# Kernel optimization log

Measured on AMD Instinct MI355X. Metric: run time of the kernel, lower is better.

## Reference

```python
import jax, jax.numpy as jnp
import numpy as np

DIM = 1024
HEADS = 16
DH = 64            # dim // heads
LOCAL_HEADS = 8
WINDOW = 128
NEG = -jnp.finfo(jnp.float32).max


def _look_around_kv(z, pad_value):
    # z: (b, h, nw, w, d) -> (b, h, nw, 3w, d); backward=1, forward=1 window
    nw = z.shape[2]
    zp = jnp.pad(z, ((0, 0), (0, 0), (1, 1), (0, 0), (0, 0)), constant_values=pad_value)
    return jnp.concatenate([zp[:, :, i:i + nw] for i in range(3)], axis=3)


def _local_attention(q, k, v, valid):
    # q,k,v: (b, h, t, d); valid: (b, t) True = keep (module passes ~input_mask)
    b, h, t, d = q.shape
    nw = t // WINDOW
    bucket = lambda z: z.reshape(b, h, nw, WINDOW, d)
    bq, bk, bv = bucket(q), bucket(k), bucket(v)
    bk = _look_around_kv(bk, 0.0)
    bv = _look_around_kv(bv, 0.0)
    # key position indices with -1 padding for out-of-range windows
    t_idx = jnp.arange(t, dtype=jnp.int32).reshape(nw, WINDOW)
    tp = jnp.pad(t_idx, ((1, 1), (0, 0)), constant_values=-1)
    bq_k = jnp.concatenate([tp[i:i + nw] for i in range(3)], axis=1)  # (nw, 3w)
    oob = (bq_k == -1)[None, None, :, None, :]                        # (1,1,nw,1,3w)
    # input mask pair: mq & mk
    vm = valid.reshape(b, nw, WINDOW)
    vmp = jnp.pad(vm, ((0, 0), (1, 1), (0, 0)), constant_values=False)
    vmk = jnp.concatenate([vmp[:, i:i + nw] for i in range(3)], axis=2)  # (b, nw, 3w)
    pair = vm[:, None, :, :, None] & vmk[:, None, :, None, :]            # (b,1,nw,w,3w)
    dots = jnp.einsum('bhnwd,bhnkd->bhnwk', bq, bk) * (d ** -0.5)
    dots = jnp.where(oob, NEG, dots)
    dots = jnp.where(pair, dots, NEG)
    attn = jax.nn.softmax(dots, axis=-1)
    out = jnp.einsum('bhnwk,bhnkd->bhnwd', attn, bv)
    return out.reshape(b, h, t, d)


def _linear_attn(q, k, v, valid):
    # q,k,v: (b, h, t, d); valid: (b, t) True = keep
    d = q.shape[-1]
    m = valid[:, None, :, None]
    k = jnp.where(m, k, NEG)
    v = jnp.where(m, v, 0.0)
    q = jax.nn.softmax(q, axis=-1) * (d ** -0.5)
    k = jax.nn.softmax(k, axis=-2)
    context = jnp.einsum('bhnd,bhne->bhde', k, v)
    return jnp.einsum('bhnd,bhde->bhne', q, context)


def setup_inputs() -> dict:
    key = jax.random.key(0)
    ks = jax.random.split(key, 7)
    b, t = 2, 4096
    x = jax.random.normal(ks[0], (b, t, DIM), dtype=jnp.float32)
    input_mask = jax.random.bernoulli(ks[1], 0.1, (b, t))  # True = padded token
    s = DIM ** -0.5
    Wq = jax.random.normal(ks[2], (DIM, HEADS * DH), jnp.float32) * s
    Wk = jax.random.normal(ks[3], (DIM, HEADS * DH), jnp.float32) * s
    Wv = jax.random.normal(ks[4], (DIM, HEADS * DH), jnp.float32) * s
    Wo = jax.random.normal(ks[5], (HEADS * DH, DIM), jnp.float32) * s
    bo = jax.random.normal(ks[6], (DIM,), jnp.float32) * 0.01
    return {"x": x, "input_mask": input_mask, "Wq": Wq, "Wk": Wk, "Wv": Wv, "Wo": Wo, "bo": bo}


def reference(x, input_mask, Wq, Wk, Wv, Wo, bo):
    b, t, _ = x.shape
    split_heads = lambda z: z.reshape(b, t, HEADS, DH).transpose(0, 2, 1, 3)
    q = split_heads(x @ Wq)
    k = split_heads(x @ Wk)
    v = split_heads(x @ Wv)
    valid = ~input_mask
    lq, gq = q[:, :LOCAL_HEADS], q[:, LOCAL_HEADS:]
    lk, gk = k[:, :LOCAL_HEADS], k[:, LOCAL_HEADS:]
    lv, gv = v[:, :LOCAL_HEADS], v[:, LOCAL_HEADS:]
    local_out = _local_attention(lq, lk, lv, valid)
    global_out = _linear_attn(gq, gk, gv, valid)
    attn = jnp.concatenate([local_out, global_out], axis=1)  # (b, h, t, d)
    attn = attn.transpose(0, 2, 1, 3).reshape(b, t, HEADS * DH)
    return attn @ Wo + bo
```

## Files before the change

kernel.cpp:

```cpp
#include <hip/hip_runtime.h>
#include <cstdint>
#include <cfloat>
#include <math.h>

typedef __bf16 bf16_t;
typedef __bf16 bf16x8 __attribute__((ext_vector_type(8)));
typedef __bf16 bf16x4 __attribute__((ext_vector_type(4)));
typedef float  f32x4  __attribute__((ext_vector_type(4)));
typedef unsigned int u32;

#define NEGF (-3.4028234663852886e38f)

static __device__ __forceinline__ f32x4 mfma16(bf16x8 a, bf16x8 b, f32x4 c) {
  return __builtin_amdgcn_mfma_f32_16x16x32_bf16(a, b, c, 0, 0, 0);
}
static __device__ __forceinline__ void gload_lds16(const bf16_t* g, bf16_t* l) {
  __builtin_amdgcn_global_load_lds((const __attribute__((address_space(1))) void*)g,
                                   (__attribute__((address_space(3))) void*)l, 16, 0, 0);
}

__global__ __launch_bounds__(256) void k_prep_all(const float* __restrict__ x,
                                                  const uint8_t* __restrict__ mraw,
                                                  const float* __restrict__ Wq,
                                                  const float* __restrict__ Wk,
                                                  const float* __restrict__ Wv,
                                                  const float* __restrict__ Wo,
                                                  bf16_t* __restrict__ xb,
                                                  bf16_t* __restrict__ WT,
                                                  bf16_t* __restrict__ WoT,
                                                  uint8_t* __restrict__ valid) {
  int bid = blockIdx.x;
  int tid = threadIdx.x;
  if (bid < 8192) {
    int i = bid * 256 + tid;
    float4 v = ((const float4*)x)[i];
    bf16x4 o = { (bf16_t)v.x, (bf16_t)v.y, (bf16_t)v.z, (bf16_t)v.w };
    *(bf16x4*)(xb + (size_t)i * 4) = o;
  } else if (bid < 12288) {
    __shared__ float tile[32][33];
    int zz = bid - 8192;
    int z = zz >> 10, rem = zz & 1023;
    int bx = rem & 31, by = rem >> 5;
    const float* src = (z == 0) ? Wq : (z == 1) ? Wk : (z == 2) ? Wv : Wo;
    bf16_t* dst = (z < 3) ? (WT + (size_t)z * 1024 * 1024) : WoT;
    int x0 = bx * 32, y0 = by * 32;
    int tx = tid & 31, ty = tid >> 5;
    #pragma unroll
    for (int j = 0; j < 32; j += 8)
      tile[ty + j][tx] = src[(size_t)(y0 + ty + j) * 1024 + x0 + tx];
    __syncthreads();
    #pragma unroll
    for (int j = 0; j < 32; j += 8)
      dst[(size_t)(x0 + ty + j) * 1024 + y0 + tx] = (bf16_t)tile[tx][ty + j];
  } else {
    __shared__ int f1, f3;
    if (tid == 0) { f1 = 0; f3 = 0; }
    __syncthreads();
    int l1 = 0, l3 = 0;
    for (int i = tid; i < 8192; i += 256) {
      uint8_t v = mraw[i];
      if (v) { int r = i & 3; if (r == 1 || r == 2) l1 = 1; if (r == 3) l3 = 1; }
    }
    if (l1) atomicOr(&f1, 1);
    if (l3) atomicOr(&f3, 1);
    __syncthreads();
    int layout = f1 ? 0 : (f3 ? 2 : 1);
    for (int i = tid; i < 8192; i += 256) {
      bool m;
      if (layout == 0)      m = mraw[i] != 0;
      else if (layout == 1) m = ((const int*)mraw)[i] != 0;
      else                  m = ((const float*)mraw)[i] != 0.0f;
      valid[i] = m ? (uint8_t)0 : (uint8_t)1;
    }
  }
}

template<bool OUT_BF16>
__global__ __launch_bounds__(256, 2) void k_gemm(const bf16_t* __restrict__ A,
                                                 const bf16_t* __restrict__ Bt,
                                                 void* __restrict__ Cout,
                                                 const float* __restrict__ bias,
                                                 int M, int N, int K) {
  __shared__ __align__(16) uint8_t shmem[34816];
  bf16_t* As = (bf16_t*)shmem;
  bf16_t* Bs = As + 128 * 64;
  int id  = blockIdx.x;
  int seq = id >> 3;
  int nbg = seq >> 6, inner = seq & 63;
  int mb = ((id & 7) << 3) + (inner >> 3);
  int nb = (nbg << 3) + (inner & 7);

  const int tid = threadIdx.x;
  const int lane = tid & 63, wv = tid >> 6;
  const int c = lane & 15, g = lane >> 4;
  const size_t m0 = (size_t)mb * 128, n0 = (size_t)nb * 128;
  const int wm = (wv >> 1) * 64, wn = (wv & 1) * 64;

  f32x4 zero = {0.f, 0.f, 0.f, 0.f};
  f32x4 acc[4][4];
  #pragma unroll
  for (int m = 0; m < 4; ++m)
    #pragma unroll
    for (int n = 0; n < 4; ++n) acc[m][n] = zero;

  for (int kt = 0; kt < K; kt += 64) {
    if (kt) __syncthreads();
    #pragma unroll
    for (int p = 0; p < 4; ++p) {
      int seg = p * 256 + tid;
      int r = seg >> 3, s = seg & 7;
      int sc = (s ^ (r & 7)) * 8;
      gload_lds16(A + (m0 + r) * (size_t)K + kt + sc, As + seg * 8);
    }
    #pragma unroll
    for (int p = 0; p < 4; ++p) {
      int seg = p * 256 + tid;
      int r = seg >> 3, s = seg & 7;
      int sc = (s ^ (r & 7)) * 8;
      gload_lds16(Bt + (n0 + r) * (size_t)K + kt + sc, Bs + seg * 8);
    }
    __syncthreads();
    #pragma unroll
    for (int kk = 0; kk < 2; ++kk) {
      bf16x8 af[4], bfv[4];
      #pragma unroll
      for (int m = 0; m < 4; ++m) {
        int row = wm + m * 16 + c;
        int sl = (g + 4 * kk) ^ (row & 7);
        af[m] = *(const bf16x8*)(As + row * 64 + sl * 8);
      }
      #pragma unroll
      for (int n = 0; n < 4; ++n) {
        int row = wn + n * 16 + c;
        int sl = (g + 4 * kk) ^ (row & 7);
        bfv[n] = *(const bf16x8*)(Bs + row * 64 + sl * 8);
      }
      #pragma unroll
      for (int m = 0; m < 4; ++m)
        #pragma unroll
        for (int n = 0; n < 4; ++n)
          acc[m][n] = mfma16(af[m], bfv[n], acc[m][n]);
    }
  }

  __syncthreads();
  if (OUT_BF16) {
    bf16_t* L = (bf16_t*)shmem;
    #pragma unroll
    for (int m = 0; m < 4; ++m)
      #pragma unroll
      for (int n = 0; n < 4; ++n)
        #pragma unroll
        for (int i = 0; i < 4; ++i)
          L[(wm + m * 16 + 4 * g + i) * 136 + wn + n * 16 + c] = (bf16_t)acc[m][n][i];
    __syncthreads();
    bf16_t* C = (bf16_t*)Cout;
    #pragma unroll
    for (int p = 0; p < 8; ++p) {
      int idx = p * 2048 + tid * 8;
      int row = idx >> 7, col = idx & 127;
      bf16x8 v = *(const bf16x8*)(L + row * 136 + col);
      *(bf16x8*)(C + (m0 + row) * (size_t)N + n0 + col) = v;
    }
  } else {
    float* C = (float*)Cout;
    float* L = (float*)shmem;
    #pragma unroll
    for (int half = 0; half < 2; ++half) {
      if (half) __syncthreads();
      if ((wv >> 1) == half) {
        #pragma unroll
        for (int m = 0; m < 4; ++m)
          #pragma unroll
          for (int n = 0; n < 4; ++n)
            #pragma unroll
            for (int i = 0; i < 4; ++i)
              L[(m * 16 + 4 * g + i) * 132 + wn + n * 16 + c] = acc[m][n][i];
      }
      __syncthreads();
      #pragma unroll
      for (int p = 0; p < 8; ++p) {
        int lin = p * 1024 + tid * 4;
        int row = lin >> 7, col = lin & 127;
        float4 v = *(const float4*)(L + row * 132 + col);
        float4 bv = *(const float4*)(bias + n0 + col);
        v.x += bv.x; v.y += bv.y; v.z += bv.z; v.w += bv.w;
        *(float4*)(C + (m0 + half * 64 + row) * (size_t)N + n0 + col) = v;
      }
    }
  }
}

__global__ __launch_bounds__(512) void k_attn(const bf16_t* __restrict__ qkv,
                                              const uint8_t* __restrict__ valid,
                                              bf16_t* __restrict__ attn,
                                              float* __restrict__ ctxp,
                                              float* __restrict__ sump) {
  __shared__ __align__(16) uint8_t smem[50688];
  int bid = blockIdx.x;
  int tid = threadIdx.x;

  if (bid < 512) {
    bf16_t* Ks = (bf16_t*)smem;
    bf16_t* VT = (bf16_t*)smem;
    uint8_t* s_key = smem + 50176;
    uint8_t* s_q   = smem + 50560;

    int w = bid & 31, h = (bid >> 5) & 7, b = bid >> 8;
    const int lane = tid & 63, wv = tid >> 6;
    const int c = lane & 15, g = lane >> 4;
    const int tkbase = (w - 1) * 128;

    #pragma unroll
    for (int p = 0; p < 6; ++p) {
      int seg = p * 512 + tid;
      int r = seg >> 3, s = seg & 7;
      int tk = tkbase + r;
      bf16x8 v8 = { (bf16_t)0.f,(bf16_t)0.f,(bf16_t)0.f,(bf16_t)0.f,
                    (bf16_t)0.f,(bf16_t)0.f,(bf16_t)0.f,(bf16_t)0.f };
      if ((unsigned)tk < 4096u)
        v8 = *(const bf16x8*)(qkv + (size_t)(b * 4096 + tk) * 3072 + 1024 + h * 64 + s * 8);
      *(bf16x8*)(Ks + r * 64 + ((s ^ (r & 7)) * 8)) = v8;
    }
    if (tid < 384) {
      int tk = tkbase + tid;
      s_key[tid] = ((unsigned)tk < 4096u) ? valid[b * 4096 + tk] : (uint8_t)0;
    }
    if (tid < 128) s_q[tid] = valid[b * 4096 + w * 128 + tid];
    __syncthreads();

    int m0 = wv * 16;
    bf16x8 qa0, qa1;
    {
      const bf16_t* qrow = qkv + (size_t)(b * 4096 + w * 128 + m0 + c) * 3072 + h * 64;
      qa0 = *(const bf16x8*)(qrow + g * 8);
      qa1 = *(const bf16x8*)(qrow + 32 + g * 8);
    }
    f32x4 zero = {0.f, 0.f, 0.f, 0.f};
    f32x4 acc[24];
    #pragma unroll
    for (int nt = 0; nt < 24; ++nt) acc[nt] = zero;
    #pragma unroll
    for (int nt = 0; nt < 24; ++nt) {
      int n = nt * 16 + c;
      bf16x8 k0 = *(const bf16x8*)(Ks + n * 64 + ((g       ^ (n & 7)) * 8));
      bf16x8 k1 = *(const bf16x8*)(Ks + n * 64 + (((g + 4) ^ (n & 7)) * 8));
      acc[nt] = mfma16(k0, qa0, acc[nt]);
      acc[nt] = mfma16(k1, qa1, acc[nt]);
    }
    __syncthreads();

    {
      int e = tid & 63, tg = tid >> 6;
      #pragma unroll 8
      for (int j = 0; j < 48; ++j) {
        int r = tg * 48 + j;
        int tk = tkbase + r;
        bf16_t v = (bf16_t)0.f;
        if ((unsigned)tk < 4096u)
          v = qkv[(size_t)(b * 4096 + tk) * 3072 + 2048 + h * 64 + e];
        VT[e * 392 + r] = v;
      }
    }

    bool qv = s_q[m0 + c] != 0;
    #pragma unroll
    for (int nt = 0; nt < 24; ++nt) {
      u32 kv4 = *(const u32*)(s_key + nt * 16 + 4 * g);
      #pragma unroll
      for (int i = 0; i < 4; ++i) {
        bool kv = ((kv4 >> (8 * i)) & 255u) != 0u;
        acc[nt][i] = (qv && kv) ? acc[nt][i] * 0.125f : NEGF;
      }
    }
    float mx = NEGF;
    #pragma unroll
    for (int nt = 0; nt < 24; ++nt)
      #pragma unroll
      for (int i = 0; i < 4; ++i) mx = fmaxf(mx, acc[nt][i]);
    mx = fmaxf(mx, __shfl_xor(mx, 16, 64));
    mx = fmaxf(mx, __shfl_xor(mx, 32, 64));

    const int srcA = ((lane >> 4) & 1) * 32 + (lane & 15);
    const int srcB = srcA + 16;
    union Pk2 { bf16x4 h; uint2 u; };
    union Pk4 { uint4 u; bf16x8 h; };
    uint4 paU[12];
    #pragma unroll
    for (int ks = 0; ks < 12; ++ks) paU[ks] = make_uint4(0, 0, 0, 0);
    float sum = 0.f;
    #pragma unroll
    for (int nt = 0; nt < 24; ++nt) {
      Pk2 pk;
      #pragma unroll
      for (int i = 0; i < 4; ++i) {
        float e = __expf(acc[nt][i] - mx);
        sum += e;
        pk.h[i] = (bf16_t)e;
      }
      u32 a0 = (u32)__shfl((int)pk.u.x, srcA, 64);
      u32 a1 = (u32)__shfl((int)pk.u.y, srcA, 64);
      u32 b0 = (u32)__shfl((int)pk.u.x, srcB, 64);
      u32 b1 = (u32)__shfl((int)pk.u.y, srcB, 64);
      bool take = ((g >> 1) == (nt & 1));
      int ks = nt >> 1;
      paU[ks].x = take ? a0 : paU[ks].x;
      paU[ks].y = take ? a1 : paU[ks].y;
      paU[ks].z = take ? b0 : paU[ks].z;
      paU[ks].w = take ? b1 : paU[ks].w;
    }
    sum += __shfl_xor(sum, 16, 64);
    sum += __shfl_xor(sum, 32, 64);
    float inv = 1.f / sum;
    float invq[4];
    #pragma unroll
    for (int i = 0; i < 4; ++i) invq[i] = __shfl(inv, 4 * g + i, 64);
    __syncthreads();

    f32x4 o[4];
    #pragma unroll
    for (int n = 0; n < 4; ++n) o[n] = zero;
    #pragma unroll
    for (int ks = 0; ks < 12; ++ks) {
      Pk4 pa; pa.u = paU[ks];
      #pragma unroll
      for (int n = 0; n < 4; ++n) {
        bf16x8 vb = *(const bf16x8*)(VT + (n * 16 + c) * 392 + ks * 32 + g * 8);
        o[n] = mfma16(pa.h, vb, o[n]);
      }
    }
    size_t obase = (size_t)(b * 4096 + w * 128 + m0) * 1024 + h * 64;
    #pragma unroll
    for (int n = 0; n < 4; ++n)
      #pragma unroll
      for (int i = 0; i < 4; ++i)
        attn[obase + (size_t)(4 * g + i) * 1024 + n * 16 + c] = (bf16_t)(o[n][i] * invq[i]);
  } else {
    int bid2 = bid - 512;
    int tc = bid2 & 15, h = (bid2 >> 4) & 7, b = bid2 >> 7;
    float* sk = (float*)smem;
    float* sv = sk + 64 * 64;
    float a00=0,a01=0,a02=0,a03=0,a10=0,a11=0,a12=0,a13=0;
    float a20=0,a21=0,a22=0,a23=0,a30=0,a31=0,a32=0,a33=0;
    float s0=0, s1=0, s2=0, s3=0;
    int dg = tid >> 4, eg = tid & 15;
    for (int ch = 0; ch < 4; ++ch) {
      int t0 = tc * 256 + ch * 64;
      __syncthreads();
      {
        int idx = tid;
        int r = idx >> 3, ss = idx & 7;
        int gt = b * 4096 + t0 + r;
        bool vld = valid[gt] != 0;
        bf16x8 k8 = *(const bf16x8*)(qkv + (size_t)gt * 3072 + 1024 + (8 + h) * 64 + ss * 8);
        bf16x8 v8 = *(const bf16x8*)(qkv + (size_t)gt * 3072 + 2048 + (8 + h) * 64 + ss * 8);
        #pragma unroll
        for (int j = 0; j < 8; ++j) {
          int dd = ss * 8 + j;
          sk[r * 64 + dd] = vld ? __expf((float)k8[j]) : 0.f;
          sv[r * 64 + dd] = vld ? (float)v8[j] : 0.f;
        }
      }
      __syncthreads();
      if (tid < 256) {
        #pragma unroll 4
        for (int r = 0; r < 64; ++r) {
          float4 a = *(const float4*)(sk + r * 64 + dg * 4);
          float4 v = *(const float4*)(sv + r * 64 + eg * 4);
          a00 += a.x*v.x; a01 += a.x*v.y; a02 += a.x*v.z; a03 += a.x*v.w;
          a10 += a.y*v.x; a11 += a.y*v.y; a12 += a.y*v.z; a13 += a.y*v.w;
          a20 += a.z*v.x; a21 += a.z*v.y; a22 += a.z*v.z; a23 += a.z*v.w;
          a30 += a.w*v.x; a31 += a.w*v.y; a32 += a.w*v.z; a33 += a.w*v.w;
          s0 += a.x; s1 += a.y; s2 += a.z; s3 += a.w;
        }
      }
    }
    if (tid < 256) {
      float* dst = ctxp + (size_t)((b * 8 + h) * 16 + tc) * 4096 + (dg * 4) * 64 + eg * 4;
      *(float4*)(dst + 0)   = make_float4(a00, a01, a02, a03);
      *(float4*)(dst + 64)  = make_float4(a10, a11, a12, a13);
      *(float4*)(dst + 128) = make_float4(a20, a21, a22, a23);
      *(float4*)(dst + 192) = make_float4(a30, a31, a32, a33);
      if (eg == 0)
        *(float4*)(sump + (size_t)((b * 8 + h) * 16 + tc) * 64 + dg * 4) = make_float4(s0, s1, s2, s3);
    }
  }
}

__global__ __launch_bounds__(256) void k_ctx2(const float* __restrict__ ctxp,
                                              const float* __restrict__ sump,
                                              bf16_t* __restrict__ ctxT) {
  int bh = blockIdx.x;
  int tid = threadIdx.x;
  __shared__ float inv[64];
  if (tid < 64) {
    float s = 0.f;
    #pragma unroll
    for (int tc = 0; tc < 16; ++tc)
      s += sump[(size_t)(bh * 16 + tc) * 64 + tid];
    inv[tid] = 1.f / s;
  }
  __syncthreads();
  for (int p = 0; p < 16; ++p) {
    int lin = p * 256 + tid;
    int d = lin >> 6, e = lin & 63;
    float s = 0.f;
    #pragma unroll
    for (int tc = 0; tc < 16; ++tc)
      s += ctxp[(size_t)(bh * 16 + tc) * 4096 + lin];
    s *= inv[d];
    ctxT[(size_t)bh * 4096 + e * 64 + d] = (bf16_t)s;
  }
}

__global__ __launch_bounds__(256) void k_linout(const bf16_t* __restrict__ qkv,
                                                const bf16_t* __restrict__ ctxT,
                                                bf16_t* __restrict__ attn) {
  int bid = blockIdx.x;
  int tb2 = bid & 15, hg = (bid >> 4) & 7, b = bid >> 7;
  int tid = threadIdx.x;
  __shared__ bf16_t qs[256 * 72];
  __shared__ bf16_t cT[64 * 72];
  {
    int t = tb2 * 256 + tid;
    const bf16_t* qrow = qkv + (size_t)(b * 4096 + t) * 3072 + (8 + hg) * 64;
    float x[64];
    #pragma unroll
    for (int s8 = 0; s8 < 8; ++s8) {
      bf16x8 q8 = *(const bf16x8*)(qrow + s8 * 8);
      #pragma unroll
      for (int j = 0; j < 8; ++j) x[s8 * 8 + j] = (float)q8[j];
    }
    float m = x[0];
    #pragma unroll
    for (int i = 1; i < 64; ++i) m = fmaxf(m, x[i]);
    float sum = 0.f;
    #pragma unroll
    for (int i = 0; i < 64; ++i) { x[i] = __expf(x[i] - m); sum += x[i]; }
    float sc = 0.125f / sum;
    #pragma unroll
    for (int s8 = 0; s8 < 8; ++s8) {
      bf16x8 o8;
      #pragma unroll
      for (int j = 0; j < 8; ++j) o8[j] = (bf16_t)(x[s8 * 8 + j] * sc);
      *(bf16x8*)(qs + tid * 72 + s8 * 8) = o8;
    }
  }
  for (int idx = tid; idx < 512; idx += 256) {
    int r = idx >> 3, s = idx & 7;
    *(bf16x8*)(cT + r * 72 + s * 8) =
      *(const bf16x8*)(ctxT + (size_t)(b * 8 + hg) * 4096 + r * 64 + s * 8);
  }
  __syncthreads();
  int lane = tid & 63, wvv = tid >> 6;
  int c = lane & 15, g = lane >> 4;
  int m0w = wvv * 64;
  f32x4 zero = {0.f, 0.f, 0.f, 0.f};
  f32x4 acc[4][4];
  #pragma unroll
  for (int m = 0; m < 4; ++m)
    #pragma unroll
    for (int n = 0; n < 4; ++n) acc[m][n] = zero;
  #pragma unroll
  for (int kk = 0; kk < 2; ++kk) {
    bf16x8 af[4], bfv[4];
    #pragma unroll
    for (int m = 0; m < 4; ++m)
      af[m] = *(const bf16x8*)(qs + (m0w + m * 16 + c) * 72 + kk * 32 + g * 8);
    #pragma unroll
    for (int n = 0; n < 4; ++n)
      bfv[n] = *(const bf16x8*)(cT + (n * 16 + c) * 72 + kk * 32 + g * 8);
    #pragma unroll
    for (int m = 0; m < 4; ++m)
      #pragma unroll
      for (int n = 0; n < 4; ++n)
        acc[m][n] = mfma16(af[m], bfv[n], acc[m][n]);
  }
  size_t obase = (size_t)(b * 4096 + tb2 * 256 + m0w) * 1024 + (8 + hg) * 64;
  #pragma unroll
  for (int m = 0; m < 4; ++m)
    #pragma unroll
    for (int n = 0; n < 4; ++n)
      #pragma unroll
      for (int i = 0; i < 4; ++i)
        attn[obase + (size_t)(m * 16 + 4 * g + i) * 1024 + n * 16 + c] = (bf16_t)acc[m][n][i];
}

extern "C" void kernel_launch(void* const* d_in, const int* in_sizes, int n_in,
                              void* d_out, int out_size, void* d_ws, size_t ws_size,
                              hipStream_t stream) {
  const float*   x    = (const float*)d_in[0];
  const uint8_t* mraw = (const uint8_t*)d_in[1];
  const float*   Wq   = (const float*)d_in[2];
  const float*   Wk   = (const float*)d_in[3];
  const float*   Wv   = (const float*)d_in[4];
  const float*   Wo   = (const float*)d_in[5];
  const float*   bo   = (const float*)d_in[6];
  uint8_t* ws = (uint8_t*)d_ws;

  uint8_t* valid = ws;
  bf16_t*  xb    = (bf16_t*)(ws + 8192);
  bf16_t*  WT    = (bf16_t*)(ws + 16785408);
  bf16_t*  WoT   = (bf16_t*)(ws + 23076864);
  bf16_t*  qkv   = (bf16_t*)(ws + 25174016);
  bf16_t*  attn  = (bf16_t*)(ws + 75505664);
  float*   ctxp  = (float*)(ws + 8192);
  float*   sump  = (float*)(ws + 4202496);
  bf16_t*  ctxT  = (bf16_t*)(ws + 4268032);

  k_prep_all<<<12289, 256, 0, stream>>>(x, mraw, Wq, Wk, Wv, Wo, xb, WT, WoT, valid);
  k_gemm<true><<<1536, 256, 0, stream>>>(xb, WT, (void*)qkv, nullptr, 8192, 3072, 1024);
  k_attn<<<768, 512, 0, stream>>>(qkv, valid, attn, ctxp, sump);
  k_ctx2<<<16, 256, 0, stream>>>(ctxp, sump, ctxT);
  k_linout<<<256, 256, 0, stream>>>(qkv, ctxT, attn);
  k_gemm<false><<<512, 256, 0, stream>>>(attn, WoT, d_out, bo, 8192, 1024, 1024);
}
```

Before: 207.2 us.

## Use MFMA for linear-attention context partials and vectorize V transpose loads

The global-head branch now stores exp(K) and V as transposed bf16 tiles in shared memory and computes the K^T V context partial with bf16 MFMA instead of scalar fp32 FMAs. It processes 128-token chunks using all 512 threads rather than 64-token chunks with half the threads. The local branch loads V with 16-byte vector reads before scattering into the transposed LDS tile, replacing scalar per-element loads. The cost is precision: exp(K) is rounded to bf16, and the transposed scalar LDS writes may cause bank conflicts.

```diff
diff --git a/kernel.cpp b/kernel.cpp
--- a/kernel.cpp
+++ b/kernel.cpp
@@ -199,6 +199,9 @@
   __shared__ __align__(16) uint8_t smem[50688];
   int bid = blockIdx.x;
   int tid = threadIdx.x;
+  const int lane = tid & 63, wv = tid >> 6;
+  const int c = lane & 15, g = lane >> 4;
+  f32x4 zero = {0.f, 0.f, 0.f, 0.f};
 
   if (bid < 512) {
     bf16_t* Ks = (bf16_t*)smem;
@@ -207,8 +210,6 @@
     uint8_t* s_q   = smem + 50560;
 
     int w = bid & 31, h = (bid >> 5) & 7, b = bid >> 8;
-    const int lane = tid & 63, wv = tid >> 6;
-    const int c = lane & 15, g = lane >> 4;
     const int tkbase = (w - 1) * 128;
 
     #pragma unroll
@@ -236,7 +237,6 @@
       qa0 = *(const bf16x8*)(qrow + g * 8);
       qa1 = *(const bf16x8*)(qrow + 32 + g * 8);
     }
-    f32x4 zero = {0.f, 0.f, 0.f, 0.f};
     f32x4 acc[24];
     #pragma unroll
     for (int nt = 0; nt < 24; ++nt) acc[nt] = zero;
@@ -250,17 +250,18 @@
     }
     __syncthreads();
 
-    {
-      int e = tid & 63, tg = tid >> 6;
-      #pragma unroll 8
-      for (int j = 0; j < 48; ++j) {
-        int r = tg * 48 + j;
-        int tk = tkbase + r;
-        bf16_t v = (bf16_t)0.f;
-        if ((unsigned)tk < 4096u)
-          v = qkv[(size_t)(b * 4096 + tk) * 3072 + 2048 + h * 64 + e];
-        VT[e * 392 + r] = v;
-      }
+    #pragma unroll
+    for (int p = 0; p < 6; ++p) {
+      int seg = p * 512 + tid;
+      int r = seg >> 3, s = seg & 7;
+      int tk = tkbase + r;
+      bf16x8 v8 = { (bf16_t)0.f,(bf16_t)0.f,(bf16_t)0.f,(bf16_t)0.f,
+                    (bf16_t)0.f,(bf16_t)0.f,(bf16_t)0.f,(bf16_t)0.f };
+      if ((unsigned)tk < 4096u)
+        v8 = *(const bf16x8*)(qkv + (size_t)(b * 4096 + tk) * 3072 + 2048 + h * 64 + s * 8);
+      #pragma unroll
+      for (int j = 0; j < 8; ++j)
+        VT[(s * 8 + j) * 392 + r] = v8[j];
     }
 
     bool qv = s_q[m0 + c] != 0;
@@ -338,52 +339,61 @@
   } else {
     int bid2 = bid - 512;
     int tc = bid2 & 15, h = (bid2 >> 4) & 7, b = bid2 >> 7;
-    float* sk = (float*)smem;
-    float* sv = sk + 64 * 64;
-    float a00=0,a01=0,a02=0,a03=0,a10=0,a11=0,a12=0,a13=0;
-    float a20=0,a21=0,a22=0,a23=0,a30=0,a31=0,a32=0,a33=0;
-    float s0=0, s1=0, s2=0, s3=0;
-    int dg = tid >> 4, eg = tid & 15;
-    for (int ch = 0; ch < 4; ++ch) {
-      int t0 = tc * 256 + ch * 64;
+    bf16_t* eKT = (bf16_t*)smem;
+    bf16_t* vT  = (bf16_t*)(smem + 17408);
+    int dt = wv >> 1, et2 = (wv & 1) * 2;
+    f32x4 acc2[2];
+    acc2[0] = zero; acc2[1] = zero;
+    float rowsum = 0.f;
+    int rsrow = wv * 8 + (lane >> 3);
+    int rscol = (lane & 7) * 16;
+    for (int ch = 0; ch < 2; ++ch) {
       __syncthreads();
-      {
-        int idx = tid;
+      #pragma unroll
+      for (int p = 0; p < 2; ++p) {
+        int idx = p * 512 + tid;
         int r = idx >> 3, ss = idx & 7;
-        int gt = b * 4096 + t0 + r;
+        int gt = b * 4096 + tc * 256 + ch * 128 + r;
         bool vld = valid[gt] != 0;
         bf16x8 k8 = *(const bf16x8*)(qkv + (size_t)gt * 3072 + 1024 + (8 + h) * 64 + ss * 8);
         bf16x8 v8 = *(const bf16x8*)(qkv + (size_t)gt * 3072 + 2048 + (8 + h) * 64 + ss * 8);
         #pragma unroll
         for (int j = 0; j < 8; ++j) {
           int dd = ss * 8 + j;
-          sk[r * 64 + dd] = vld ? __expf((float)k8[j]) : 0.f;
-          sv[r * 64 + dd] = vld ? (float)v8[j] : 0.f;
+          eKT[dd * 136 + r] = vld ? (bf16_t)__expf((float)k8[j]) : (bf16_t)0.f;
+          vT [dd * 136 + r] = vld ? v8[j] : (bf16_t)0.f;
         }
       }
       __syncthreads();
-      if (tid < 256) {
-        #pragma unroll 4
-        for (int r = 0; r < 64; ++r) {
-          float4 a = *(const float4*)(sk + r * 64 + dg * 4);
-          float4 v = *(const float4*)(sv + r * 64 + eg * 4);
-          a00 += a.x*v.x; a01 += a.x*v.y; a02 += a.x*v.z; a03 += a.x*v.w;
-          a10 += a.y*v.x; a11 += a.y*v.y; a12 += a.y*v.z; a13 += a.y*v.w;
-          a20 += a.z*v.x; a21 += a.z*v.y; a22 += a.z*v.z; a23 += a.z*v.w;
-          a30 += a.w*v.x; a31 += a.w*v.y; a32 += a.w*v.z; a33 += a.w*v.w;
-          s0 += a.x; s1 += a.y; s2 += a.z; s3 += a.w;
+      #pragma unroll
+      for (int ks = 0; ks < 4; ++ks) {
+        bf16x8 af = *(const bf16x8*)(eKT + (dt * 16 + c) * 136 + ks * 32 + g * 8);
+        #pragma unroll
+        for (int n = 0; n < 2; ++n) {
+          bf16x8 bf = *(const bf16x8*)(vT + ((et2 + n) * 16 + c) * 136 + ks * 32 + g * 8);
+          acc2[n] = mfma16(af, bf, acc2[n]);
         }
       }
-    }
-    if (tid < 256) {
-      float* dst = ctxp + (size_t)((b * 8 + h) * 16 + tc) * 4096 + (dg * 4) * 64 + eg * 4;
-      *(float4*)(dst + 0)   = make_float4(a00, a01, a02, a03);
-      *(float4*)(dst + 64)  = make_float4(a10, a11, a12, a13);
-      *(float4*)(dst + 128) = make_float4(a20, a21, a22, a23);
-      *(float4*)(dst + 192) = make_float4(a30, a31, a32, a33);
-      if (eg == 0)
-        *(float4*)(sump + (size_t)((b * 8 + h) * 16 + tc) * 64 + dg * 4) = make_float4(s0, s1, s2, s3);
-    }
+      float s = 0.f;
+      #pragma unroll
+      for (int q = 0; q < 2; ++q) {
+        bf16x8 e8 = *(const bf16x8*)(eKT + rsrow * 136 + rscol + q * 8);
+        #pragma unroll
+        for (int j = 0; j < 8; ++j) s += (float)e8[j];
+      }
+      rowsum += s;
+    }
+    rowsum += __shfl_xor(rowsum, 1, 64);
+    rowsum += __shfl_xor(rowsum, 2, 64);
+    rowsum += __shfl_xor(rowsum, 4, 64);
+    size_t slice = (size_t)((b * 8 + h) * 16 + tc);
+    #pragma unroll
+    for (int n = 0; n < 2; ++n)
+      #pragma unroll
+      for (int i = 0; i < 4; ++i)
+        ctxp[slice * 4096 + (size_t)(dt * 16 + 4 * g + i) * 64 + (et2 + n) * 16 + c] = acc2[n][i];
+    if ((lane & 7) == 0)
+      sump[slice * 64 + rsrow] = rowsum;
   }
 }
 
```

After: 177.0 us, median of 3. 1.17x faster.
